# Kernel tuning notes

Hardware: AMD Instinct MI355X
Metric: run time of the kernel (lower is better)

Reference implementation:

```python
import jax, jax.numpy as jnp
import numpy as np

HIDDEN = 1024
HEADS = 16
HEAD_DIM = HIDDEN // HEADS
B, S = 2, 2048


def setup_inputs() -> dict:
    key = jax.random.key(0)
    k1, k2, k3 = jax.random.split(key, 3)
    x = jax.random.normal(k1, (B, S, HIDDEN), dtype=jnp.float32)
    qkv_w = jax.random.normal(k2, (3 * HIDDEN, HIDDEN), dtype=jnp.float32) * (HIDDEN ** -0.5)
    out_w = jax.random.normal(k3, (HIDDEN, HIDDEN), dtype=jnp.float32) * (HIDDEN ** -0.5)
    return {"x": x, "qkv_w": qkv_w, "out_w": out_w}


def reference(x, qkv_w, out_w):
    b, s, d = x.shape
    scale = HEAD_DIM ** -0.5
    # qkv projection (Linear without bias: x @ W^T)
    qkv = x @ qkv_w.T                                   # [b, s, 3d]
    qkv = qkv.reshape(b, s, 3, HEADS, HEAD_DIM)
    qkv = jnp.transpose(qkv, (2, 0, 3, 1, 4))           # [3, b, h, s, hd]
    q, k, v = qkv[0] * scale, qkv[1], qkv[2]
    # causal attention (blocked torch loop == full causal softmax attention)
    scores = jnp.einsum('bhqd,bhkd->bhqk', q, k)        # [b, h, s, s]
    causal = jnp.tril(jnp.ones((s, s), dtype=bool))
    scores = jnp.where(causal[None, None], scores, -jnp.inf)
    weights = jax.nn.softmax(scores, axis=-1)
    attn = jnp.einsum('bhqk,bhkd->bhqd', weights, v)    # [b, h, s, hd]
    attn = jnp.transpose(attn, (0, 2, 1, 3)).reshape(b, s, d)
    return attn @ out_w.T
```

## Files before the change

### kernel.cpp

```cpp
#include <hip/hip_runtime.h>
#include <hip/hip_bf16.h>
#include <math.h>

#define HIDDEN 1024
#define HEADS 16
#define HDIM 64
#define BATCH 2
#define SEQ 2048
#define BHN (BATCH*HEADS)
#define MTOT (BATCH*SEQ)

typedef __attribute__((ext_vector_type(8))) short short8;
typedef __attribute__((ext_vector_type(4))) short short4v;
typedef __attribute__((ext_vector_type(4))) float floatx4;

#define GL2LDS(gsrc, ldst) __builtin_amdgcn_global_load_lds( \
    (const __attribute__((address_space(1))) void*)(gsrc), \
    (__attribute__((address_space(3))) void*)(ldst), 16, 0, 0)

__device__ __forceinline__ short f2bf(float f) {
  union { float f; unsigned u; } v; v.f = f;
  unsigned u = v.u;
  unsigned r = (u + 0x7fffu + ((u >> 16) & 1u)) >> 16;
  return (short)r;
}

__global__ __launch_bounds__(256) void cvt3_f32_bf16(
    const float* __restrict__ a, const float* __restrict__ b, const float* __restrict__ c,
    short* __restrict__ oa, short* __restrict__ ob, short* __restrict__ oc) {
  int i = blockIdx.x * 256 + threadIdx.x;
  const float* src; short* dst; int j;
  if (i < 1048576)      { src = a; dst = oa; j = i; }
  else if (i < 1835008) { src = b; dst = ob; j = i - 1048576; }
  else                  { src = c; dst = oc; j = i - 1835008; }
  float4 f = reinterpret_cast<const float4*>(src)[j];
  short4 o;
  o.x = f2bf(f.x); o.y = f2bf(f.y); o.z = f2bf(f.z); o.w = f2bf(f.w);
  reinterpret_cast<short4*>(dst)[j] = o;
}

template<int EPI, int BN>
__global__ __launch_bounds__(256) void gemm_bt(
    const short* __restrict__ A, const short* __restrict__ B,
    int M, int N, int K,
    float* __restrict__ outF,
    short* __restrict__ outQ, short* __restrict__ outK, short* __restrict__ outV)
{
  constexpr int WN = BN / 2;
  constexpr int NI = BN / 32;
  __shared__ __align__(16) short As[128*64];
  __shared__ __align__(16) short Bs[BN*64];
  const int tid = threadIdx.x;
  const int wv = tid >> 6;
  const int lane = tid & 63;
  const int l15 = lane & 15;
  const int quad = lane >> 4;
  const int swl = l15 & 7;
  const int wm = wv >> 1, wn = wv & 1;
  const int row0 = blockIdx.y * 128, col0 = blockIdx.x * BN;

  floatx4 acc[4][NI];
#pragma unroll
  for (int i = 0; i < 4; i++)
#pragma unroll
    for (int j = 0; j < NI; j++) acc[i][j] = (floatx4){0.f, 0.f, 0.f, 0.f};

  for (int k0 = 0; k0 < K; k0 += 64) {
#pragma unroll
    for (int rd = 0; rd < 4; ++rd) {
      int chunk = rd * 256 + tid;
      int r = chunk >> 3, c = ((chunk & 7) ^ (r & 7)) << 3;
      GL2LDS(A + (long)(row0 + r) * K + k0 + c, As + (rd * 256 + wv * 64) * 8);
    }
#pragma unroll
    for (int rd = 0; rd < BN / 32; ++rd) {
      int chunk = rd * 256 + tid;
      int r = chunk >> 3, c = ((chunk & 7) ^ (r & 7)) << 3;
      GL2LDS(B + (long)(col0 + r) * K + k0 + c, Bs + (rd * 256 + wv * 64) * 8);
    }
    __syncthreads();

    short8 af[4][2], bfr[NI][2];
#pragma unroll
    for (int mi = 0; mi < 4; mi++) {
      const short* ap = As + (wm * 64 + mi * 16 + l15) * 64;
#pragma unroll
      for (int kk = 0; kk < 2; kk++)
        af[mi][kk] = *(const short8*)(ap + (((kk * 4 + quad) ^ swl) << 3));
    }
#pragma unroll
    for (int ni = 0; ni < NI; ni++) {
      const short* bp = Bs + (wn * WN + ni * 16 + l15) * 64;
#pragma unroll
      for (int kk = 0; kk < 2; kk++)
        bfr[ni][kk] = *(const short8*)(bp + (((kk * 4 + quad) ^ swl) << 3));
    }
#pragma unroll
    for (int mi = 0; mi < 4; mi++)
#pragma unroll
      for (int ni = 0; ni < NI; ni++)
#pragma unroll
        for (int kk = 0; kk < 2; kk++)
          acc[mi][ni] = __builtin_amdgcn_mfma_f32_16x16x32_bf16(af[mi][kk], bfr[ni][kk], acc[mi][ni], 0, 0, 0);
    __syncthreads();
  }

  if (EPI == 2) {
#pragma unroll
    for (int mi = 0; mi < 4; mi++) {
      int rr = row0 + wm * 64 + mi * 16 + quad * 4;
#pragma unroll
      for (int ni = 0; ni < NI; ni++) {
        int cc = col0 + wn * WN + ni * 16 + l15;
#pragma unroll
        for (int r = 0; r < 4; r++)
          outF[(long)(rr + r) * N + cc] = acc[mi][ni][r];
      }
    }
  } else {
#pragma unroll
    for (int mi = 0; mi < 4; mi++) {
      int rowg = row0 + wm * 64 + mi * 16 + quad * 4;
#pragma unroll
      for (int ni = 0; ni < NI; ni++) {
        int j = col0 + wn * WN + ni * 16 + l15;
        int t = j >> 10;
        int rem = j & 1023;
        int h = rem >> 6, d = rem & 63;
#pragma unroll
        for (int r = 0; r < 4; r++) {
          int i = rowg + r;
          int b = i >> 11, s = i & 2047;
          int bh = b * HEADS + h;
          float v = acc[mi][ni][r];
          if (t == 0)      outQ[(bh * SEQ + s) * HDIM + d] = f2bf(v * 0.18033688011112042f);
          else if (t == 1) outK[(bh * SEQ + s) * HDIM + d] = f2bf(v);
          else             outV[(bh * HDIM + d) * SEQ + s] = f2bf(v);
        }
      }
    }
  }
}

__device__ __forceinline__ void stage_kv(const short* __restrict__ kg,
                                         const short* __restrict__ vT,
                                         int bh, int kt, short* KsB, short* VsB,
                                         int tid, int wv) {
#pragma unroll
  for (int i = 0; i < 2; ++i) {
    int slot = i * 256 + tid;
    int r = slot >> 3;
    int c = ((slot & 7) ^ (r & 7)) << 3;
    GL2LDS(kg + (bh * SEQ + kt * 64 + r) * HDIM + c, KsB + (i * 256 + wv * 64) * 8);
    GL2LDS(vT + (bh * HDIM + r) * SEQ + kt * 64 + c, VsB + (i * 256 + wv * 64) * 8);
  }
}

__global__ __launch_bounds__(256, 4) void flash_attn(
    const short* __restrict__ qg, const short* __restrict__ kg,
    const short* __restrict__ vT, short* __restrict__ attn)
{
  __shared__ __align__(16) short Ks[2][64 * 64];
  __shared__ __align__(16) short Vs[2][64 * 64];

  const int tid = threadIdx.x;
  const int wv = tid >> 6, lane = tid & 63;
  const int l15 = lane & 15, quad = lane >> 4;
  const int bh = blockIdx.x;
  const int yl = (int)blockIdx.y;
  const int sgrp = yl >> 3, y0 = yl & 7;
  const int yp = ((sgrp >> 1) << 4) + ((sgrp & 1) ? (15 - y0) : y0);
  const int rt = 31 - yp;
  const int m0 = rt * 64 + wv * 16;
  const int swl = l15 & 7;

  short8 aq[2];
  {
    const short* qp = qg + (long)(bh * SEQ + m0 + l15) * HDIM + quad * 8;
    aq[0] = *(const short8*)qp;
    aq[1] = *(const short8*)(qp + 32);
  }

  const short ONE = (short)0x3F80;
  const short4v ones4 = {ONE, ONE, ONE, ONE};

  floatx4 o[4], lsum = (floatx4){0.f, 0.f, 0.f, 0.f};
#pragma unroll
  for (int nt = 0; nt < 4; nt++) o[nt] = (floatx4){0.f, 0.f, 0.f, 0.f};

  const int ntiles = rt + 1;
  stage_kv(kg, vT, bh, 0, Ks[0], Vs[0], tid, wv);

  for (int kt = 0; kt < ntiles; ++kt) {
    __syncthreads();
    const int buf = kt & 1;
    if (kt + 1 < ntiles)
      stage_kv(kg, vT, bh, kt + 1, Ks[buf ^ 1], Vs[buf ^ 1], tid, wv);

    const short* KsB = Ks[buf];
    const short* VsB = Vs[buf];

    floatx4 sc4[4];
#pragma unroll
    for (int nh = 0; nh < 4; nh++) sc4[nh] = (floatx4){0.f, 0.f, 0.f, 0.f};
#pragma unroll
    for (int nh = 0; nh < 4; nh++) {
      const short* kp = KsB + (nh * 16 + l15) * 64;
      short8 kf0 = *(const short8*)(kp + ((quad ^ swl) << 3));
      short8 kf1 = *(const short8*)(kp + (((4 + quad) ^ swl) << 3));
      sc4[nh] = __builtin_amdgcn_mfma_f32_16x16x32_bf16(kf0, aq[0], sc4[nh], 0, 0, 0);
      sc4[nh] = __builtin_amdgcn_mfma_f32_16x16x32_bf16(kf1, aq[1], sc4[nh], 0, 0, 0);
    }

    short4v pa[4];
    const int qrow = m0 + l15;
    const bool full = (kt * 64 + 63) <= m0;
#pragma unroll
    for (int nh = 0; nh < 4; nh++) {
      unsigned u[4];
#pragma unroll
      for (int r = 0; r < 4; r++) {
        float pe = __builtin_amdgcn_exp2f(sc4[nh][r]);
        if (!full) {
          const int kpos = kt * 64 + nh * 16 + quad * 4 + r;
          pe = (kpos <= qrow) ? pe : 0.f;
        }
        u[r] = __builtin_bit_cast(unsigned, pe) & 0xffff0000u;
      }
      uint2 w;
      w.x = (u[0] >> 16) | u[1];
      w.y = (u[2] >> 16) | u[3];
      pa[nh] = __builtin_bit_cast(short4v, w);
    }

#pragma unroll
    for (int kk = 0; kk < 4; kk++) {
      short4v bv[4];
#pragma unroll
      for (int nt = 0; nt < 4; nt++) {
        const int ch = (kk * 2 + (quad >> 1)) ^ swl;
        bv[nt] = *(const short4v*)(VsB + (nt * 16 + l15) * 64 + (ch << 3) + ((quad & 1) << 2));
      }
      lsum = __builtin_amdgcn_mfma_f32_16x16x16bf16_1k(pa[kk], ones4, lsum, 0, 0, 0);
#pragma unroll
      for (int nt = 0; nt < 4; nt++)
        o[nt] = __builtin_amdgcn_mfma_f32_16x16x16bf16_1k(pa[kk], bv[nt], o[nt], 0, 0, 0);
    }
  }

  const int b = bh >> 4, h = bh & 15;
#pragma unroll
  for (int r = 0; r < 4; r++) {
    const float inv = 1.0f / lsum[r];
    const int srow = m0 + quad * 4 + r;
#pragma unroll
    for (int nt = 0; nt < 4; nt++)
      attn[(long)(b * SEQ + srow) * HIDDEN + h * HDIM + nt * 16 + l15] = f2bf(o[nt][r] * inv);
  }
}

extern "C" void kernel_launch(void* const* d_in, const int* in_sizes, int n_in,
                              void* d_out, int out_size, void* d_ws, size_t ws_size,
                              hipStream_t stream) {
  const float* x     = (const float*)d_in[0];
  const float* qkv_w = (const float*)d_in[1];
  const float* out_w = (const float*)d_in[2];
  float* out = (float*)d_out;

  short* xb   = (short*)d_ws;
  short* wqb  = xb  + MTOT * HIDDEN;
  short* wob  = wqb + 3 * HIDDEN * HIDDEN;
  short* qB   = wob + HIDDEN * HIDDEN;
  short* kB   = qB  + BHN * SEQ * HDIM;
  short* vTB  = kB  + BHN * SEQ * HDIM;
  short* attn = vTB + BHN * SEQ * HDIM;

  cvt3_f32_bf16<<<dim3(8192), dim3(256), 0, stream>>>(x, qkv_w, out_w, xb, wqb, wob);

  gemm_bt<1, 128><<<dim3(3 * HIDDEN / 128, MTOT / 128), dim3(256), 0, stream>>>(
      xb, wqb, MTOT, 3 * HIDDEN, HIDDEN, nullptr, qB, kB, vTB);

  flash_attn<<<dim3(BHN, SEQ / 64), dim3(256), 0, stream>>>(qB, kB, vTB, attn);

  gemm_bt<2, 64><<<dim3(HIDDEN / 64, MTOT / 128), dim3(256), 0, stream>>>(
      attn, wob, MTOT, HIDDEN, HIDDEN, out, nullptr, nullptr, nullptr);
}
```

Measured before the change: 176.3 us.

## Add 256x256 double-buffered QKV GEMM and MFMA priority hints in attention

Replaces the 128x128 QKV projection GEMM with a dedicated 512-thread kernel. It uses 256x256 tiles and double-buffers LDS through direct global-to-LDS loads, which raises data reuse per loaded tile and overlaps the next tile's load with compute. It also wraps the MFMA sections in both the new GEMM and flash attention with s_setprio so a wave holds issue priority while running its matrix ops. In exchange, the new GEMM needs 128KB of LDS per block and launches only 192 blocks, which may leave many CUs idle and limits occupancy.

```diff
diff --git a/kernel.cpp b/kernel.cpp
--- a/kernel.cpp
+++ b/kernel.cpp
@@ -37,6 +37,95 @@
   short4 o;
   o.x = f2bf(f.x); o.y = f2bf(f.y); o.z = f2bf(f.z); o.w = f2bf(f.w);
   reinterpret_cast<short4*>(dst)[j] = o;
+}
+
+__device__ __forceinline__ void stage256(const short* __restrict__ A, const short* __restrict__ B,
+                                         int row0, int col0, int k0,
+                                         short* Asb, short* Bsb, int tid, int wv) {
+#pragma unroll
+  for (int ld = 0; ld < 4; ++ld) {
+    int chunk = ld * 512 + tid;
+    int r = chunk >> 3;
+    int c = ((chunk & 7) ^ (r & 7)) << 3;
+    GL2LDS(A + (long)(row0 + r) * 1024 + k0 + c, Asb + (ld * 512 + wv * 64) * 8);
+    GL2LDS(B + (long)(col0 + r) * 1024 + k0 + c, Bsb + (ld * 512 + wv * 64) * 8);
+  }
+}
+
+__global__ __launch_bounds__(512, 2) void gemm_qkv256(
+    const short* __restrict__ A, const short* __restrict__ B,
+    short* __restrict__ outQ, short* __restrict__ outK, short* __restrict__ outV)
+{
+  __shared__ __align__(16) short As[2][256 * 64];
+  __shared__ __align__(16) short Bs[2][256 * 64];
+  const int tid = threadIdx.x;
+  const int wv = tid >> 6, lane = tid & 63;
+  const int l15 = lane & 15, quad = lane >> 4;
+  const int swl = l15 & 7;
+  const int wr = wv >> 2, wc = wv & 3;
+  const int row0 = blockIdx.y * 256, col0 = blockIdx.x * 256;
+
+  floatx4 acc[8][4];
+#pragma unroll
+  for (int i = 0; i < 8; i++)
+#pragma unroll
+    for (int j = 0; j < 4; j++) acc[i][j] = (floatx4){0.f, 0.f, 0.f, 0.f};
+
+  int buf = 0;
+  stage256(A, B, row0, col0, 0, As[0], Bs[0], tid, wv);
+
+  for (int t = 0; t < 16; ++t) {
+    __syncthreads();
+    if (t + 1 < 16)
+      stage256(A, B, row0, col0, (t + 1) * 64, As[buf ^ 1], Bs[buf ^ 1], tid, wv);
+
+    const short* Ab = As[buf];
+    const short* Bb = Bs[buf];
+#pragma unroll
+    for (int kk = 0; kk < 2; ++kk) {
+      short8 bfr[4];
+#pragma unroll
+      for (int ni = 0; ni < 4; ++ni)
+        bfr[ni] = *(const short8*)(Bb + (wc * 64 + ni * 16 + l15) * 64 + (((kk * 4 + quad) ^ swl) << 3));
+#pragma unroll
+      for (int mh = 0; mh < 2; ++mh) {
+        short8 af[4];
+#pragma unroll
+        for (int a = 0; a < 4; ++a)
+          af[a] = *(const short8*)(Ab + (wr * 128 + mh * 64 + a * 16 + l15) * 64 + (((kk * 4 + quad) ^ swl) << 3));
+        __builtin_amdgcn_s_setprio(1);
+#pragma unroll
+        for (int a = 0; a < 4; ++a)
+#pragma unroll
+          for (int ni = 0; ni < 4; ++ni)
+            acc[mh * 4 + a][ni] = __builtin_amdgcn_mfma_f32_16x16x32_bf16(af[a], bfr[ni], acc[mh * 4 + a][ni], 0, 0, 0);
+        __builtin_amdgcn_s_setprio(0);
+      }
+    }
+    buf ^= 1;
+  }
+
+#pragma unroll
+  for (int mi = 0; mi < 8; ++mi) {
+    int rowg = row0 + wr * 128 + mi * 16 + quad * 4;
+#pragma unroll
+    for (int ni = 0; ni < 4; ++ni) {
+      int j = col0 + wc * 64 + ni * 16 + l15;
+      int tt = j >> 10;
+      int rem = j & 1023;
+      int h = rem >> 6, d = rem & 63;
+#pragma unroll
+      for (int r = 0; r < 4; ++r) {
+        int i = rowg + r;
+        int b = i >> 11, s = i & 2047;
+        int bh = b * HEADS + h;
+        float v = acc[mi][ni][r];
+        if (tt == 0)      outQ[(bh * SEQ + s) * HDIM + d] = f2bf(v * 0.18033688011112042f);
+        else if (tt == 1) outK[(bh * SEQ + s) * HDIM + d] = f2bf(v);
+        else              outV[(bh * HDIM + d) * SEQ + s] = f2bf(v);
+      }
+    }
+  }
 }
 
 template<int EPI, int BN>
@@ -117,28 +206,6 @@
           outF[(long)(rr + r) * N + cc] = acc[mi][ni][r];
       }
     }
-  } else {
-#pragma unroll
-    for (int mi = 0; mi < 4; mi++) {
-      int rowg = row0 + wm * 64 + mi * 16 + quad * 4;
-#pragma unroll
-      for (int ni = 0; ni < NI; ni++) {
-        int j = col0 + wn * WN + ni * 16 + l15;
-        int t = j >> 10;
-        int rem = j & 1023;
-        int h = rem >> 6, d = rem & 63;
-#pragma unroll
-        for (int r = 0; r < 4; r++) {
-          int i = rowg + r;
-          int b = i >> 11, s = i & 2047;
-          int bh = b * HEADS + h;
-          float v = acc[mi][ni][r];
-          if (t == 0)      outQ[(bh * SEQ + s) * HDIM + d] = f2bf(v * 0.18033688011112042f);
-          else if (t == 1) outK[(bh * SEQ + s) * HDIM + d] = f2bf(v);
-          else             outV[(bh * HDIM + d) * SEQ + s] = f2bf(v);
-        }
-      }
-    }
   }
 }
 
@@ -203,6 +270,7 @@
     floatx4 sc4[4];
 #pragma unroll
     for (int nh = 0; nh < 4; nh++) sc4[nh] = (floatx4){0.f, 0.f, 0.f, 0.f};
+    __builtin_amdgcn_s_setprio(1);
 #pragma unroll
     for (int nh = 0; nh < 4; nh++) {
       const short* kp = KsB + (nh * 16 + l15) * 64;
@@ -211,6 +279,7 @@
       sc4[nh] = __builtin_amdgcn_mfma_f32_16x16x32_bf16(kf0, aq[0], sc4[nh], 0, 0, 0);
       sc4[nh] = __builtin_amdgcn_mfma_f32_16x16x32_bf16(kf1, aq[1], sc4[nh], 0, 0, 0);
     }
+    __builtin_amdgcn_s_setprio(0);
 
     short4v pa[4];
     const int qrow = m0 + l15;
@@ -233,6 +302,7 @@
       pa[nh] = __builtin_bit_cast(short4v, w);
     }
 
+    __builtin_amdgcn_s_setprio(1);
 #pragma unroll
     for (int kk = 0; kk < 4; kk++) {
       short4v bv[4];
@@ -246,6 +316,7 @@
       for (int nt = 0; nt < 4; nt++)
         o[nt] = __builtin_amdgcn_mfma_f32_16x16x16bf16_1k(pa[kk], bv[nt], o[nt], 0, 0, 0);
     }
+    __builtin_amdgcn_s_setprio(0);
   }
 
   const int b = bh >> 4, h = bh & 15;
@@ -277,8 +348,8 @@
 
   cvt3_f32_bf16<<<dim3(8192), dim3(256), 0, stream>>>(x, qkv_w, out_w, xb, wqb, wob);
 
-  gemm_bt<1, 128><<<dim3(3 * HIDDEN / 128, MTOT / 128), dim3(256), 0, stream>>>(
-      xb, wqb, MTOT, 3 * HIDDEN, HIDDEN, nullptr, qB, kB, vTB);
+  gemm_qkv256<<<dim3(3 * HIDDEN / 256, MTOT / 256), dim3(512), 0, stream>>>(
+      xb, wqb, qB, kB, vTB);
 
   flash_attn<<<dim3(BHN, SEQ / 64), dim3(256), 0, stream>>>(qB, kB, vTB, attn);
 
```

New measurement: 202.1 us. 1.15x slower.

## Split flash attention waves into 2x2 query/key grid with LDS reduction

Applied to the files above, without the earlier changes.

Each wave now handles 32 query rows over half of every 64-key tile, instead of 16 query rows over the full tile. K and V fragments loaded from LDS are reused across two query groups, which cuts LDS read traffic per MFMA. At the end, the partial outputs and row sums of the two key halves are combined through shared memory. The change also adds s_setprio around the MFMA sections, and costs more accumulator registers plus an extra reduction step with two barriers.

```diff
diff --git a/kernel.cpp b/kernel.cpp
--- a/kernel.cpp
+++ b/kernel.cpp
@@ -171,22 +171,29 @@
   const int sgrp = yl >> 3, y0 = yl & 7;
   const int yp = ((sgrp >> 1) << 4) + ((sgrp & 1) ? (15 - y0) : y0);
   const int rt = 31 - yp;
-  const int m0 = rt * 64 + wv * 16;
+  const int qh = wv >> 1;
+  const int kh = wv & 1;
+  const int m0 = rt * 64 + qh * 32;
   const int swl = l15 & 7;
 
-  short8 aq[2];
-  {
-    const short* qp = qg + (long)(bh * SEQ + m0 + l15) * HDIM + quad * 8;
-    aq[0] = *(const short8*)qp;
-    aq[1] = *(const short8*)(qp + 32);
+  short8 aq[2][2];
+#pragma unroll
+  for (int g = 0; g < 2; g++) {
+    const short* qp = qg + (long)(bh * SEQ + m0 + g * 16 + l15) * HDIM + quad * 8;
+    aq[g][0] = *(const short8*)qp;
+    aq[g][1] = *(const short8*)(qp + 32);
   }
 
   const short ONE = (short)0x3F80;
   const short4v ones4 = {ONE, ONE, ONE, ONE};
 
-  floatx4 o[4], lsum = (floatx4){0.f, 0.f, 0.f, 0.f};
-#pragma unroll
-  for (int nt = 0; nt < 4; nt++) o[nt] = (floatx4){0.f, 0.f, 0.f, 0.f};
+  floatx4 o[2][4], lsum[2];
+#pragma unroll
+  for (int g = 0; g < 2; g++) {
+    lsum[g] = (floatx4){0.f, 0.f, 0.f, 0.f};
+#pragma unroll
+    for (int nt = 0; nt < 4; nt++) o[g][nt] = (floatx4){0.f, 0.f, 0.f, 0.f};
+  }
 
   const int ntiles = rt + 1;
   stage_kv(kg, vT, bh, 0, Ks[0], Vs[0], tid, wv);
@@ -200,62 +207,106 @@
     const short* KsB = Ks[buf];
     const short* VsB = Vs[buf];
 
-    floatx4 sc4[4];
-#pragma unroll
-    for (int nh = 0; nh < 4; nh++) sc4[nh] = (floatx4){0.f, 0.f, 0.f, 0.f};
-#pragma unroll
-    for (int nh = 0; nh < 4; nh++) {
-      const short* kp = KsB + (nh * 16 + l15) * 64;
+    floatx4 sc[2][2];
+#pragma unroll
+    for (int g = 0; g < 2; g++)
+#pragma unroll
+      for (int sub = 0; sub < 2; sub++) sc[g][sub] = (floatx4){0.f, 0.f, 0.f, 0.f};
+    __builtin_amdgcn_s_setprio(1);
+#pragma unroll
+    for (int sub = 0; sub < 2; sub++) {
+      const short* kp = KsB + (kh * 32 + sub * 16 + l15) * 64;
       short8 kf0 = *(const short8*)(kp + ((quad ^ swl) << 3));
       short8 kf1 = *(const short8*)(kp + (((4 + quad) ^ swl) << 3));
-      sc4[nh] = __builtin_amdgcn_mfma_f32_16x16x32_bf16(kf0, aq[0], sc4[nh], 0, 0, 0);
-      sc4[nh] = __builtin_amdgcn_mfma_f32_16x16x32_bf16(kf1, aq[1], sc4[nh], 0, 0, 0);
-    }
-
-    short4v pa[4];
-    const int qrow = m0 + l15;
-    const bool full = (kt * 64 + 63) <= m0;
-#pragma unroll
-    for (int nh = 0; nh < 4; nh++) {
-      unsigned u[4];
+#pragma unroll
+      for (int g = 0; g < 2; g++) {
+        sc[g][sub] = __builtin_amdgcn_mfma_f32_16x16x32_bf16(kf0, aq[g][0], sc[g][sub], 0, 0, 0);
+        sc[g][sub] = __builtin_amdgcn_mfma_f32_16x16x32_bf16(kf1, aq[g][1], sc[g][sub], 0, 0, 0);
+      }
+    }
+    __builtin_amdgcn_s_setprio(0);
+
+    short4v pa[2][2];
+#pragma unroll
+    for (int g = 0; g < 2; g++) {
+      const int qrow = m0 + g * 16 + l15;
+#pragma unroll
+      for (int sub = 0; sub < 2; sub++) {
+        const int kbase = kt * 64 + kh * 32 + sub * 16;
+        const bool full = (kbase + 15) <= (m0 + g * 16);
+        unsigned u[4];
+#pragma unroll
+        for (int r = 0; r < 4; r++) {
+          float pe = __builtin_amdgcn_exp2f(sc[g][sub][r]);
+          if (!full) {
+            const int kpos = kbase + quad * 4 + r;
+            pe = (kpos <= qrow) ? pe : 0.f;
+          }
+          u[r] = __builtin_bit_cast(unsigned, pe) & 0xffff0000u;
+        }
+        uint2 w;
+        w.x = (u[0] >> 16) | u[1];
+        w.y = (u[2] >> 16) | u[3];
+        pa[g][sub] = __builtin_bit_cast(short4v, w);
+      }
+    }
+
+    __builtin_amdgcn_s_setprio(1);
+#pragma unroll
+    for (int sub = 0; sub < 2; sub++) {
+      short4v bv[4];
+#pragma unroll
+      for (int nt = 0; nt < 4; nt++) {
+        const int ch = (kh * 4 + sub * 2 + (quad >> 1)) ^ swl;
+        bv[nt] = *(const short4v*)(VsB + (nt * 16 + l15) * 64 + (ch << 3) + ((quad & 1) << 2));
+      }
+#pragma unroll
+      for (int g = 0; g < 2; g++) {
+        lsum[g] = __builtin_amdgcn_mfma_f32_16x16x16bf16_1k(pa[g][sub], ones4, lsum[g], 0, 0, 0);
+#pragma unroll
+        for (int nt = 0; nt < 4; nt++)
+          o[g][nt] = __builtin_amdgcn_mfma_f32_16x16x16bf16_1k(pa[g][sub], bv[nt], o[g][nt], 0, 0, 0);
+      }
+    }
+    __builtin_amdgcn_s_setprio(0);
+  }
+
+  __syncthreads();
+  float* redO = (float*)&Ks[0][0];
+  float* redL = (float*)&Vs[0][0];
+  if (kh == 1) {
+#pragma unroll
+    for (int g = 0; g < 2; g++) {
+      const int base = (qh * 64 + lane) * 2 + g;
+#pragma unroll
+      for (int nt = 0; nt < 4; nt++)
+#pragma unroll
+        for (int r = 0; r < 4; r++)
+          redO[base * 16 + nt * 4 + r] = o[g][nt][r];
+#pragma unroll
+      for (int r = 0; r < 4; r++) redL[base * 4 + r] = lsum[g][r];
+    }
+  }
+  __syncthreads();
+  if (kh == 0) {
+    const int b = bh >> 4, h = bh & 15;
+#pragma unroll
+    for (int g = 0; g < 2; g++) {
+      const int base = (qh * 64 + lane) * 2 + g;
+      floatx4 lt = lsum[g];
+#pragma unroll
+      for (int r = 0; r < 4; r++) lt[r] += redL[base * 4 + r];
 #pragma unroll
       for (int r = 0; r < 4; r++) {
-        float pe = __builtin_amdgcn_exp2f(sc4[nh][r]);
-        if (!full) {
-          const int kpos = kt * 64 + nh * 16 + quad * 4 + r;
-          pe = (kpos <= qrow) ? pe : 0.f;
+        const float inv = 1.0f / lt[r];
+        const int srow = m0 + g * 16 + quad * 4 + r;
+#pragma unroll
+        for (int nt = 0; nt < 4; nt++) {
+          float val = o[g][nt][r] + redO[base * 16 + nt * 4 + r];
+          attn[(long)(b * SEQ + srow) * HIDDEN + h * HDIM + nt * 16 + l15] = f2bf(val * inv);
         }
-        u[r] = __builtin_bit_cast(unsigned, pe) & 0xffff0000u;
-      }
-      uint2 w;
-      w.x = (u[0] >> 16) | u[1];
-      w.y = (u[2] >> 16) | u[3];
-      pa[nh] = __builtin_bit_cast(short4v, w);
-    }
-
-#pragma unroll
-    for (int kk = 0; kk < 4; kk++) {
-      short4v bv[4];
-#pragma unroll
-      for (int nt = 0; nt < 4; nt++) {
-        const int ch = (kk * 2 + (quad >> 1)) ^ swl;
-        bv[nt] = *(const short4v*)(VsB + (nt * 16 + l15) * 64 + (ch << 3) + ((quad & 1) << 2));
-      }
-      lsum = __builtin_amdgcn_mfma_f32_16x16x16bf16_1k(pa[kk], ones4, lsum, 0, 0, 0);
-#pragma unroll
-      for (int nt = 0; nt < 4; nt++)
-        o[nt] = __builtin_amdgcn_mfma_f32_16x16x16bf16_1k(pa[kk], bv[nt], o[nt], 0, 0, 0);
-    }
-  }
-
-  const int b = bh >> 4, h = bh & 15;
-#pragma unroll
-  for (int r = 0; r < 4; r++) {
-    const float inv = 1.0f / lsum[r];
-    const int srow = m0 + quad * 4 + r;
-#pragma unroll
-    for (int nt = 0; nt < 4; nt++)
-      attn[(long)(b * SEQ + srow) * HIDDEN + h * HDIM + nt * 16 + l15] = f2bf(o[nt][r] * inv);
+      }
+    }
   }
 }
 
```

Result: no change. 173.6 us (-1.5%).
